# Performance work log

Measured on AMD Instinct MI355X. Metric: run time of the kernel, lower is better.

## Reference

```python
import jax, jax.numpy as jnp
import numpy as np


def _perm_mats():
    E = np.zeros((36, 9), np.float32)
    D = np.zeros((9, 36), np.float32)
    c = 0
    for i in range(8):
        for j in range(i + 1, 9):
            E[c, i] = 1.0
            E[c, j] = 1.0
            D[i, c] = 1.0
            D[j, c] = 1.0
            c += 1
    assert c == 36
    return E, D


def setup_inputs() -> dict:
    key = jax.random.key(0)
    B = 32768
    # binary candidate mask: [B, 9 digits, 9 rows, 9 cols]
    mask = jnp.round(jax.random.uniform(key, (B, 9, 9, 9), dtype=jnp.float32))
    E, D = _perm_mats()
    return {"mask": mask, "enc": jnp.asarray(E), "dec": jnp.asarray(D)}


def _nn_compare(x, v):
    # NNCompare: triangular bump == 1 exactly when x == v (for integer-valued x)
    return jnp.minimum(jax.nn.relu(x - (v - 1.0)), jax.nn.relu((v + 1.0) - x))


def _nn_and(x, y):
    return jnp.clip(jnp.minimum(x, y), 0.0, 1.0)


def reference(mask, enc, dec):
    B = mask.shape[0]
    # encode_permutations: 1x1 conv 9 -> 36 (pair selection)
    perms = jnp.einsum('oc,bchw->bohw', enc, mask)          # [B,36,9,9]
    perms = _nn_compare(perms, 2.0)                          # cell contains exactly this pair
    # sum_all_permutations: 1x1 conv 36 -> 1, then == 1
    sum_p = _nn_compare(jnp.sum(perms, axis=1, keepdims=True), 1.0)  # [B,1,9,9]
    perms = _nn_and(perms, sum_p)                            # broadcast over 36 channels
    # box downsample: grouped 3x3 stride-3 sum conv
    down = perms.reshape(B, 36, 3, 3, 3, 3).sum(axis=(3, 5))  # [B,36,3,3]
    down = _nn_compare(down, 2.0)                              # exactly two such cells in box
    up = jnp.repeat(jnp.repeat(down, 3, axis=2), 3, axis=3)    # [B,36,9,9]
    up = _nn_and(up, 1.0 - perms)                              # other cells in the box
    # decode_permutations: 1x1 conv 36 -> 9
    erase = jnp.einsum('oc,bchw->bohw', dec, up)               # [B,9,9,9]
    return _nn_and(mask, 1.0 - erase)
```

## Files before the change

kernel.cpp:

```cpp
#include <hip/hip_runtime.h>
#include <stdint.h>


#define NB 8
#define NCELL (NB * 81)
#define NBOX (NB * 9)
#define CPT 3

__global__ __launch_bounds__(256) void sudoku_naked_pair_kernel(
    const float* __restrict__ mask, float* __restrict__ out) {
  __shared__ unsigned short pairm[NCELL];
  __shared__ unsigned short erls[NCELL];

  const int tid = threadIdx.x;
  const size_t base = (size_t)blockIdx.x * (NB * 729);

  uint32_t mycell[CPT];

#pragma unroll
  for (int it = 0; it < CPT; ++it) {
    const int c = tid + it * 256;
    if (c < NCELL) {
      const int b = c / 81, cell = c - b * 81;
      const float* p = mask + base + b * 729 + cell;
      uint32_t m = 0;
#pragma unroll
      for (int d = 0; d < 9; ++d) m |= (p[d * 81] != 0.0f ? 1u : 0u) << d;
      mycell[it] = m;
      pairm[c] = (unsigned short)((__popc(m) == 2) ? m : 0u);
    }
  }
  __syncthreads();

  if (tid < NBOX) {
    const int b = tid / 9, bi = tid - b * 9;
    const int bb = b * 81 + (bi / 3) * 27 + (bi % 3) * 3;
    uint32_t pm[9];
#pragma unroll
    for (int j = 0; j < 3; ++j) {
      pm[3 * j + 0] = pairm[bb + 9 * j + 0];
      pm[3 * j + 1] = pairm[bb + 9 * j + 1];
      pm[3 * j + 2] = pairm[bb + 9 * j + 2];
    }
    bool naked[9];
#pragma unroll
    for (int j = 0; j < 9; ++j) {
      int cnt = 0;
#pragma unroll
      for (int k = 0; k < 9; ++k) cnt += (pm[k] == pm[j]);
      naked[j] = (pm[j] != 0u) && (cnt == 2);
    }
#pragma unroll
    for (int j = 0; j < 9; ++j) {
      uint32_t er = 0;
#pragma unroll
      for (int k = 0; k < 9; ++k)
        if (naked[k] && pm[k] != pm[j]) er |= pm[k];
      const int cell = bb + 9 * (j / 3) + (j % 3);
      erls[cell] = (unsigned short)er;
    }
  }
  __syncthreads();

#pragma unroll
  for (int it = 0; it < CPT; ++it) {
    const int c = tid + it * 256;
    if (c < NCELL) {
      const int b = c / 81, cell = c - b * 81;
      const uint32_t fin = mycell[it] & ~(uint32_t)erls[c];
      float* q = out + base + b * 729 + cell;
#pragma unroll
      for (int d = 0; d < 9; ++d) q[d * 81] = (float)((fin >> d) & 1u);
    }
  }
}

extern "C" void kernel_launch(void* const* d_in, const int* in_sizes, int n_in,
                              void* d_out, int out_size, void* d_ws, size_t ws_size,
                              hipStream_t stream) {
  const float* mask = (const float*)d_in[0];
  float* out = (float*)d_out;
  const int B = in_sizes[0] / 729;
  const int grid = B / NB;
  sudoku_naked_pair_kernel<<<grid, 256, 0, stream>>>(mask, out);
}
```

Measured before the change: 176.6 us.

## Assign one thread per 3x3 box, dropping shared memory and barriers

The kernel now gives each thread one sudoku box. The thread loads 27 triples of floats (3 consecutive cells per digit-row), builds the masks, finds naked pairs and writes the result, all in registers. This removes the shared-memory staging, both __syncthreads and the idle threads in the middle phase. In exchange, memory accesses become strided 12-byte per-thread loads. Adjacent threads touch different boxes, so coalescing may suffer, and register pressure rises from the 27 f3 values held per thread.

```diff
diff --git a/kernel.cpp b/kernel.cpp
--- a/kernel.cpp
+++ b/kernel.cpp
@@ -2,77 +2,67 @@
 #include <stdint.h>
 
 
-#define NB 8
-#define NCELL (NB * 81)
-#define NBOX (NB * 9)
-#define CPT 3
+struct f3 { float x, y, z; };
 
-__global__ __launch_bounds__(256) void sudoku_naked_pair_kernel(
+__global__ __launch_bounds__(128) void sudoku_naked_pair_kernel(
     const float* __restrict__ mask, float* __restrict__ out) {
-  __shared__ unsigned short pairm[NCELL];
-  __shared__ unsigned short erls[NCELL];
+  const int g = blockIdx.x * 128 + threadIdx.x;
+  const int batch = g / 9, bi = g - batch * 9;
+  const size_t base = (size_t)batch * 729 + (bi / 3) * 27 + (bi % 3) * 3;
 
-  const int tid = threadIdx.x;
-  const size_t base = (size_t)blockIdx.x * (NB * 729);
+  f3 arr[9][3];
+#pragma unroll
+  for (int d = 0; d < 9; ++d)
+#pragma unroll
+    for (int j = 0; j < 3; ++j)
+      arr[d][j] = *reinterpret_cast<const f3*>(mask + base + d * 81 + j * 9);
 
-  uint32_t mycell[CPT];
+  uint32_t m[9];
+#pragma unroll
+  for (int c = 0; c < 9; ++c) m[c] = 0u;
+#pragma unroll
+  for (int d = 0; d < 9; ++d)
+#pragma unroll
+    for (int j = 0; j < 3; ++j) {
+      m[j * 3 + 0] |= (arr[d][j].x != 0.0f ? 1u : 0u) << d;
+      m[j * 3 + 1] |= (arr[d][j].y != 0.0f ? 1u : 0u) << d;
+      m[j * 3 + 2] |= (arr[d][j].z != 0.0f ? 1u : 0u) << d;
+    }
+
+  uint32_t pm[9];
+#pragma unroll
+  for (int c = 0; c < 9; ++c)
+    pm[c] = (__popc(m[c]) == 2) ? m[c] : 0u;
+
+  bool naked[9];
+#pragma unroll
+  for (int c = 0; c < 9; ++c) {
+    int cnt = 0;
+#pragma unroll
+    for (int k = 0; k < 9; ++k) cnt += (pm[k] == pm[c]);
+    naked[c] = (pm[c] != 0u) && (cnt == 2);
+  }
+
+  uint32_t fin[9];
+#pragma unroll
+  for (int c = 0; c < 9; ++c) {
+    uint32_t er = 0;
+#pragma unroll
+    for (int k = 0; k < 9; ++k)
+      if (naked[k] && pm[k] != pm[c]) er |= pm[k];
+    fin[c] = m[c] & ~er;
+  }
 
 #pragma unroll
-  for (int it = 0; it < CPT; ++it) {
-    const int c = tid + it * 256;
-    if (c < NCELL) {
-      const int b = c / 81, cell = c - b * 81;
-      const float* p = mask + base + b * 729 + cell;
-      uint32_t m = 0;
-#pragma unroll
-      for (int d = 0; d < 9; ++d) m |= (p[d * 81] != 0.0f ? 1u : 0u) << d;
-      mycell[it] = m;
-      pairm[c] = (unsigned short)((__popc(m) == 2) ? m : 0u);
-    }
-  }
-  __syncthreads();
-
-  if (tid < NBOX) {
-    const int b = tid / 9, bi = tid - b * 9;
-    const int bb = b * 81 + (bi / 3) * 27 + (bi % 3) * 3;
-    uint32_t pm[9];
+  for (int d = 0; d < 9; ++d)
 #pragma unroll
     for (int j = 0; j < 3; ++j) {
-      pm[3 * j + 0] = pairm[bb + 9 * j + 0];
-      pm[3 * j + 1] = pairm[bb + 9 * j + 1];
-      pm[3 * j + 2] = pairm[bb + 9 * j + 2];
+      f3 w;
+      w.x = (float)((fin[j * 3 + 0] >> d) & 1u);
+      w.y = (float)((fin[j * 3 + 1] >> d) & 1u);
+      w.z = (float)((fin[j * 3 + 2] >> d) & 1u);
+      *reinterpret_cast<f3*>(out + base + d * 81 + j * 9) = w;
     }
-    bool naked[9];
-#pragma unroll
-    for (int j = 0; j < 9; ++j) {
-      int cnt = 0;
-#pragma unroll
-      for (int k = 0; k < 9; ++k) cnt += (pm[k] == pm[j]);
-      naked[j] = (pm[j] != 0u) && (cnt == 2);
-    }
-#pragma unroll
-    for (int j = 0; j < 9; ++j) {
-      uint32_t er = 0;
-#pragma unroll
-      for (int k = 0; k < 9; ++k)
-        if (naked[k] && pm[k] != pm[j]) er |= pm[k];
-      const int cell = bb + 9 * (j / 3) + (j % 3);
-      erls[cell] = (unsigned short)er;
-    }
-  }
-  __syncthreads();
-
-#pragma unroll
-  for (int it = 0; it < CPT; ++it) {
-    const int c = tid + it * 256;
-    if (c < NCELL) {
-      const int b = c / 81, cell = c - b * 81;
-      const uint32_t fin = mycell[it] & ~(uint32_t)erls[c];
-      float* q = out + base + b * 729 + cell;
-#pragma unroll
-      for (int d = 0; d < 9; ++d) q[d * 81] = (float)((fin >> d) & 1u);
-    }
-  }
 }
 
 extern "C" void kernel_launch(void* const* d_in, const int* in_sizes, int n_in,
@@ -81,6 +71,7 @@
   const float* mask = (const float*)d_in[0];
   float* out = (float*)d_out;
   const int B = in_sizes[0] / 729;
-  const int grid = B / NB;
-  sudoku_naked_pair_kernel<<<grid, 256, 0, stream>>>(mask, out);
+  const int nbox = B * 9;
+  const int grid = nbox / 128;
+  sudoku_naked_pair_kernel<<<grid, 128, 0, stream>>>(mask, out);
 }
```

New measurement: 181.0 us. +2.5%, slower.
